# Kernel optimization log

Measured on AMD Instinct MI355X. Metric: run time of the kernel, lower is better.

The kernel has to match this reference:

```python
import jax, jax.numpy as jnp
import numpy as np

B, H, W, C = 2, 96, 96, 96
GROUPS = 32
EPS = 1e-5


def group_norm_dim1(x, gamma, beta):
    # Faithful to torch nn.GroupNorm(32, C) applied to an NHWC tensor:
    # dim 1 (H) is treated as the channel axis, normalized over (H//G, W, C) per group.
    b, h, w, c = x.shape
    xg = x.reshape(b, GROUPS, h // GROUPS, w, c)
    mean = xg.mean(axis=(2, 3, 4), keepdims=True)
    var = xg.var(axis=(2, 3, 4), keepdims=True)
    xn = ((xg - mean) * jax.lax.rsqrt(var + EPS)).reshape(b, h, w, c)
    return xn * gamma[None, :, None, None] + beta[None, :, None, None]


def setup_inputs() -> dict:
    key = jax.random.key(0)
    ks = jax.random.split(key, 9)
    s = 1.0 / np.sqrt(C)  # kaiming-uniform-ish scale
    x = jax.random.normal(ks[0], (B, H, W, C), dtype=jnp.float32)
    Wq = jax.random.uniform(ks[1], (C, C), jnp.float32, -s, s)
    Wk = jax.random.uniform(ks[2], (C, C), jnp.float32, -s, s)
    Wv = jax.random.uniform(ks[3], (C, C), jnp.float32, -s, s)
    Wp = jax.random.uniform(ks[4], (C, C), jnp.float32, -s, s)
    return {
        "x": x,
        "gamma": jnp.ones((H,), jnp.float32),   # GroupNorm affine weight (over dim 1)
        "beta": jnp.zeros((H,), jnp.float32),
        "Wq": Wq, "bq": jnp.zeros((C,), jnp.float32),
        "Wk": Wk, "bk": jnp.zeros((C,), jnp.float32),
        "Wv": Wv, "bv": jnp.zeros((C,), jnp.float32),
        "Wp": Wp, "bp": jnp.zeros((C,), jnp.float32),
    }


def reference(x, gamma, beta, Wq, bq, Wk, bk, Wv, bv, Wp, bp):
    b, h, w, c = x.shape
    hn = group_norm_dim1(x, gamma, beta)
    q = hn @ Wq + bq  # [B,H,W,C], Nin = contract last dim
    k = hn @ Wk + bk
    v = hn @ Wv + bv
    scale = c ** (-0.5)
    # full dense spatial attention: [B, HW, HW]
    scores = jnp.einsum('bxyc,buvc->bxyuv', q, k) * scale
    attn = jax.nn.softmax(scores.reshape(b, h, w, h * w), axis=-1).reshape(b, h, w, h, w)
    o = jnp.einsum('bxyuv,buvc->bxyc', attn, v)
    return x + (o @ Wp + bp)
```

## Files before the change

### kernel.cpp

```cpp
#include <hip/hip_runtime.h>
#include <hip/hip_bf16.h>
#include <stdint.h>

#define B_   2
#define H_   96
#define W_   96
#define C_   96
#define HW_  (H_ * W_)
#define NT_  (B_ * HW_)
#define EPS_ 1e-5f
#define KSPLIT  8
#define KRANGE  (HW_ / KSPLIT)
#define ATT_NIT (KRANGE / 32)
#define SCL (0.10206207261596575f * 1.4426950408889634f)

typedef __hip_bfloat16 bf16;
typedef __attribute__((ext_vector_type(8))) short short8;
typedef __attribute__((ext_vector_type(16))) float f32x16;

__device__ __forceinline__ uint32_t pk_bf16(float a, float b) {
    uint32_t ua = __float_as_uint(a) + 0x8000u;
    uint32_t ub = __float_as_uint(b) + 0x8000u;
    return __builtin_amdgcn_perm(ub, ua, 0x07060302u);
}
__device__ __forceinline__ float bl(uint32_t u) { uint32_t x = u << 16;         return *(float*)&x; }
__device__ __forceinline__ float bh(uint32_t u) { uint32_t x = u & 0xffff0000u; return *(float*)&x; }
__device__ __forceinline__ float fexp2(float x) { return __builtin_amdgcn_exp2f(x); }
__device__ __forceinline__ short8 lds_frag(const short* p) {
    union { int2 h[2]; short8 v; } t;
    t.h[0] = *(const int2*)(p);
    t.h[1] = *(const int2*)(p + 4);
    return t.v;
}

__device__ __forceinline__ void load_hn_frags(
        const float* __restrict__ x, const float2* __restrict__ stats,
        const float* __restrict__ gamma, const float* __restrict__ beta,
        int token, int hh, short8* hf) {
    int b = token / HW_;
    int h = (token % HW_) / W_;
    float2 st = stats[b * 32 + h / 3];
    float g0 = gamma[h];
    float ga = g0 * st.y;
    float be = beta[h] - st.x * st.y * g0;
    const float* xr = x + (size_t)token * C_ + hh * 8;
    #pragma unroll
    for (int s = 0; s < 6; ++s) {
        float4 a = *(const float4*)(xr + s * 16);
        float4 c = *(const float4*)(xr + s * 16 + 4);
        union { uint32_t w[4]; short8 v; } f;
        f.w[0] = pk_bf16(a.x * ga + be, a.y * ga + be);
        f.w[1] = pk_bf16(a.z * ga + be, a.w * ga + be);
        f.w[2] = pk_bf16(c.x * ga + be, c.y * ga + be);
        f.w[3] = pk_bf16(c.z * ga + be, c.w * ga + be);
        hf[s] = f.v;
    }
}

__global__ __launch_bounds__(1024)
void stats_prep_kernel(const float* __restrict__ x, float2* __restrict__ stats,
                       const float* __restrict__ Wq, const float* __restrict__ Wk,
                       const float* __restrict__ Wv, const float* __restrict__ Wp,
                       bf16* __restrict__ wqt, bf16* __restrict__ wkt,
                       bf16* __restrict__ wvt, bf16* __restrict__ wpt) {
    int blk = blockIdx.x;
    int tid = threadIdx.x;
    if (blk >= 64) {
        int wsel = blk - 64;
        const float* S = (wsel == 0) ? Wq : (wsel == 1) ? Wk : (wsel == 2) ? Wv : Wp;
        bf16* D = (wsel == 0) ? wqt : (wsel == 1) ? wkt : (wsel == 2) ? wvt : wpt;
        for (int i = tid; i < C_ * C_; i += 1024) {
            int r = i / C_, c = i % C_;
            D[c * C_ + r] = __float2bfloat16(S[r * C_ + c]);
        }
        return;
    }
    int b = blk >> 5, g = blk & 31;
    const int n4 = 3 * W_ * C_ / 4;
    const float4* xb = (const float4*)(x + (size_t)(b * H_ + 3 * g) * (W_ * C_));
    float s = 0.f, ss = 0.f;
    for (int i = tid; i < n4; i += 1024) {
        float4 v = xb[i];
        s  += v.x + v.y + v.z + v.w;
        ss += v.x * v.x + v.y * v.y + v.z * v.z + v.w * v.w;
    }
    #pragma unroll
    for (int off = 1; off < 64; off <<= 1) {
        s  += __shfl_xor(s, off, 64);
        ss += __shfl_xor(ss, off, 64);
    }
    __shared__ float rs[16], rss[16];
    int wid = tid >> 6;
    if ((tid & 63) == 0) { rs[wid] = s; rss[wid] = ss; }
    __syncthreads();
    if (tid == 0) {
        float ts = 0.f, tss = 0.f;
        #pragma unroll
        for (int i = 0; i < 16; ++i) { ts += rs[i]; tss += rss[i]; }
        const float n = 3 * W_ * C_;
        float mean = ts / n;
        float var  = tss / n - mean * mean;
        stats[blk] = make_float2(mean, rsqrtf(var + EPS_));
    }
}

__global__ __launch_bounds__(256)
void qkv_kernel(const float* __restrict__ x, const float2* __restrict__ stats,
                const float* __restrict__ gamma, const float* __restrict__ beta,
                const bf16* __restrict__ wqt, const bf16* __restrict__ wkt,
                const bf16* __restrict__ wvt,
                const float* __restrict__ bq, const float* __restrict__ bk,
                const float* __restrict__ bv,
                bf16* __restrict__ qb, bf16* __restrict__ kb, bf16* __restrict__ vt) {
    int blk = blockIdx.x;
    int w = blk / 144, grp = blk % 144;
    int wave = threadIdx.x >> 6, lane = threadIdx.x & 63;
    int tile = grp * 4 + wave;
    int n0 = tile * 32;
    int col = lane & 31, hh = lane >> 5;
    int token = n0 + col;

    short8 hf[6];
    load_hn_frags(x, stats, gamma, beta, token, hh, hf);

    if (w == 2) {
        int bb = n0 / HW_, nl0 = n0 % HW_;
        #pragma unroll
        for (int t = 0; t < 3; ++t) {
            int c = t * 32 + col;
            const bf16* wrow = wvt + (size_t)c * C_ + hh * 8;
            f32x16 acc = (f32x16)(0.f);
            #pragma unroll
            for (int s = 0; s < 6; ++s)
                acc = __builtin_amdgcn_mfma_f32_32x32x16_bf16(
                        hf[s], *(const short8*)(wrow + s * 16), acc, 0, 0, 0);
            float bias = bv[c];
            bf16* dst = vt + ((size_t)bb * C_ + c) * HW_ + nl0 + 4 * hh;
            #pragma unroll
            for (int g = 0; g < 4; ++g) {
                uint2 pk = make_uint2(pk_bf16(acc[4 * g] + bias, acc[4 * g + 1] + bias),
                                      pk_bf16(acc[4 * g + 2] + bias, acc[4 * g + 3] + bias));
                *(uint2*)(dst + 8 * g) = pk;
            }
        }
    } else {
        const bf16*  wt   = (w == 0) ? wqt : wkt;
        const float* bias = (w == 0) ? bq : bk;
        bf16*        dst  = (w == 0) ? qb : kb;
        float        scl  = (w == 0) ? SCL : 1.f;
        #pragma unroll
        for (int t = 0; t < 3; ++t) {
            const bf16* wrow = wt + (size_t)(t * 32 + col) * C_ + hh * 8;
            f32x16 acc = (f32x16)(0.f);
            #pragma unroll
            for (int s = 0; s < 6; ++s)
                acc = __builtin_amdgcn_mfma_f32_32x32x16_bf16(
                        *(const short8*)(wrow + s * 16), hf[s], acc, 0, 0, 0);
            #pragma unroll
            for (int g = 0; g < 4; ++g) {
                int nb = t * 32 + 8 * g + 4 * hh;
                float4 b4 = *(const float4*)(bias + nb);
                float v0 = (acc[4 * g]     + b4.x) * scl;
                float v1 = (acc[4 * g + 1] + b4.y) * scl;
                float v2 = (acc[4 * g + 2] + b4.z) * scl;
                float v3 = (acc[4 * g + 3] + b4.w) * scl;
                uint2 pk = make_uint2(pk_bf16(v0, v1), pk_bf16(v2, v3));
                *(uint2*)(dst + (size_t)token * C_ + nb) = pk;
            }
        }
    }
}

__global__ __launch_bounds__(256, 4)
void attn_kernel(const bf16* __restrict__ qb, const bf16* __restrict__ kb,
                 const bf16* __restrict__ vt,
                 bf16* __restrict__ pob, float* __restrict__ pl) {
    __shared__ short Kbuf[2][32 * 100];
    __shared__ short Vbuf[2][96 * 36];

    int blk = blockIdx.x;
    int ks = blk & 7, qg = blk >> 3;
    int b = qg / 72, g72 = qg % 72;
    int n0 = g72 * 128;
    int tid = threadIdx.x;
    int wave = tid >> 6, lane = tid & 63;
    int col = lane & 31, hh = lane >> 5;

    const bf16* kbb = kb + ((size_t)b * HW_ + (size_t)ks * KRANGE) * C_;
    const bf16* vbb = vt + (size_t)b * C_ * HW_ + (size_t)ks * KRANGE;

    int n = n0 + wave * 32 + col;
    short8 qf[6];
    {
        const bf16* qrow = qb + (size_t)(b * HW_ + n) * C_ + hh * 8;
        #pragma unroll
        for (int s = 0; s < 6; ++s) qf[s] = *(const short8*)(qrow + s * 16);
    }

    f32x16 oa[3];
    #pragma unroll
    for (int t = 0; t < 3; ++t) oa[t] = (f32x16)(0.f);
    float l_run = 0.f;

    bool isK = (tid < 128);
    int t128 = tid & 127;
    int ldsA[3], ldsB[3], goff[3];
    #pragma unroll
    for (int j = 0; j < 3; ++j) {
        int c = t128 + 128 * j;
        if (isK) {
            ldsA[j] = (c / 12) * 100 + (c % 12) * 8;
            ldsB[j] = ldsA[j] + 4;
            goff[j] = c * 8;
        } else {
            int rw = c >> 2, g = c & 3;
            ldsA[j] = rw * 36 + (2 * g - (g & 1)) * 4;
            ldsB[j] = rw * 36 + (2 * g + 2 - (g & 1)) * 4;
            goff[j] = rw * HW_ + g * 8;
        }
    }
    const bf16* gbase = isK ? kbb : vbb;
    const int itstep = isK ? (32 * C_) : 32;

    {
        short* sb = isK ? Kbuf[0] : Vbuf[0];
        #pragma unroll
        for (int j = 0; j < 3; ++j) {
            int4 r = *(const int4*)(gbase + goff[j]);
            *(int2*)(sb + ldsA[j]) = make_int2(r.x, r.y);
            *(int2*)(sb + ldsB[j]) = make_int2(r.z, r.w);
        }
    }
    __syncthreads();

    union FU { uint32_t w[4]; short8 v; };

    for (int it = 0; it < ATT_NIT; ++it) {
        int cur = it & 1;
        bool pre = (it + 1 < ATT_NIT);
        int4 r0, r1, r2;
        if (pre) {
            const bf16* g = gbase + (size_t)(it + 1) * itstep;
            r0 = *(const int4*)(g + goff[0]);
            r1 = *(const int4*)(g + goff[1]);
            r2 = *(const int4*)(g + goff[2]);
        }

        const short* Kc = Kbuf[cur];
        const short* Vc = Vbuf[cur];

        short8 kf[6];
        #pragma unroll
        for (int s = 0; s < 6; ++s)
            kf[s] = lds_frag(Kc + col * 100 + s * 16 + hh * 8);

        f32x16 st = (f32x16)(0.f);
        #pragma unroll
        for (int s = 0; s < 6; ++s)
            st = __builtin_amdgcn_mfma_f32_32x32x16_bf16(kf[s], qf[s], st, 0, 0, 0);

        float p[16], ls = 0.f;
        #pragma unroll
        for (int i = 0; i < 16; ++i) { p[i] = fexp2(st[i]); ls += p[i]; }
        l_run += ls;
        FU f0, f1;
        #pragma unroll
        for (int j = 0; j < 4; ++j) {
            f0.w[j] = pk_bf16(p[2 * j],     p[2 * j + 1]);
            f1.w[j] = pk_bf16(p[8 + 2 * j], p[8 + 2 * j + 1]);
        }

        #pragma unroll
        for (int t = 0; t < 3; ++t) {
            const short* vr = Vc + (32 * t + col) * 36 + hh * 8;
            short8 vf0 = lds_frag(vr);
            short8 vf1 = lds_frag(vr + 16);
            oa[t] = __builtin_amdgcn_mfma_f32_32x32x16_bf16(vf0, f0.v, oa[t], 0, 0, 0);
            oa[t] = __builtin_amdgcn_mfma_f32_32x32x16_bf16(vf1, f1.v, oa[t], 0, 0, 0);
        }

        if (pre) {
            short* sb = isK ? Kbuf[cur ^ 1] : Vbuf[cur ^ 1];
            *(int2*)(sb + ldsA[0]) = make_int2(r0.x, r0.y);
            *(int2*)(sb + ldsB[0]) = make_int2(r0.z, r0.w);
            *(int2*)(sb + ldsA[1]) = make_int2(r1.x, r1.y);
            *(int2*)(sb + ldsB[1]) = make_int2(r1.z, r1.w);
            *(int2*)(sb + ldsA[2]) = make_int2(r2.x, r2.y);
            *(int2*)(sb + ldsB[2]) = make_int2(r2.z, r2.w);
        }
        __syncthreads();
    }

    {
        size_t bq = (size_t)b * HW_ + n;
        float lt = l_run + __shfl_xor(l_run, 32, 64);
        if (hh == 0) pl[(size_t)ks * NT_ + bq] = lt;
        #pragma unroll
        for (int t = 0; t < 3; ++t)
            #pragma unroll
            for (int g = 0; g < 4; ++g) {
                int c0 = t * 32 + 8 * g + 4 * hh;
                uint2 pk = make_uint2(
                    pk_bf16(oa[t][4 * g],     oa[t][4 * g + 1]),
                    pk_bf16(oa[t][4 * g + 2], oa[t][4 * g + 3]));
                *(uint2*)(pob + ((size_t)ks * NT_ + bq) * C_ + c0) = pk;
            }
    }
}

__global__ __launch_bounds__(256)
void out_kernel(const float* __restrict__ x,
                const bf16* __restrict__ pob, const float* __restrict__ pl,
                const bf16* __restrict__ wpt, const float* __restrict__ bp,
                float* __restrict__ out) {
    __shared__ short ofs[32 * 100];
    __shared__ float linv_s[32];

    int tile = blockIdx.x;
    int n0 = tile * 32;
    int tid = threadIdx.x;

    if (tid < 32) {
        int token = n0 + tid;
        float l = 0.f;
        #pragma unroll
        for (int ksp = 0; ksp < KSPLIT; ++ksp) l += pl[(size_t)ksp * NT_ + token];
        linv_s[tid] = 1.f / l;
    }
    __syncthreads();

    for (int pos = tid; pos < 384; pos += 256) {
        int token = pos / 12, c8 = (pos % 12) * 8;
        float acc[8] = {0.f, 0.f, 0.f, 0.f, 0.f, 0.f, 0.f, 0.f};
        #pragma unroll
        for (int ksp = 0; ksp < KSPLIT; ++ksp) {
            uint4 u = *(const uint4*)(pob + ((size_t)ksp * NT_ + n0 + token) * C_ + c8);
            acc[0] += bl(u.x); acc[1] += bh(u.x);
            acc[2] += bl(u.y); acc[3] += bh(u.y);
            acc[4] += bl(u.z); acc[5] += bh(u.z);
            acc[6] += bl(u.w); acc[7] += bh(u.w);
        }
        float inv = linv_s[token];
        short* dst = ofs + token * 100 + c8;
        *(int2*)(dst)     = make_int2(pk_bf16(acc[0] * inv, acc[1] * inv),
                                      pk_bf16(acc[2] * inv, acc[3] * inv));
        *(int2*)(dst + 4) = make_int2(pk_bf16(acc[4] * inv, acc[5] * inv),
                                      pk_bf16(acc[6] * inv, acc[7] * inv));
    }
    __syncthreads();

    int wave = tid >> 6;
    if (wave >= 3) return;
    int lane = tid & 63, col = lane & 31, hh = lane >> 5;
    int t = wave;
    int token = n0 + col;

    short8 of[6];
    #pragma unroll
    for (int s = 0; s < 6; ++s)
        of[s] = lds_frag(ofs + col * 100 + s * 16 + hh * 8);

    f32x16 acc = (f32x16)(0.f);
    const bf16* wrow = wpt + (size_t)(t * 32 + col) * C_ + hh * 8;
    #pragma unroll
    for (int s = 0; s < 6; ++s)
        acc = __builtin_amdgcn_mfma_f32_32x32x16_bf16(
                *(const short8*)(wrow + s * 16), of[s], acc, 0, 0, 0);
    #pragma unroll
    for (int g = 0; g < 4; ++g) {
        int nb = t * 32 + 8 * g + 4 * hh;
        float4 b4 = *(const float4*)(bp + nb);
        float4 xv = *(const float4*)(x + (size_t)token * C_ + nb);
        float4 rr;
        rr.x = xv.x + acc[4 * g]     + b4.x;
        rr.y = xv.y + acc[4 * g + 1] + b4.y;
        rr.z = xv.z + acc[4 * g + 2] + b4.z;
        rr.w = xv.w + acc[4 * g + 3] + b4.w;
        *(float4*)(out + (size_t)token * C_ + nb) = rr;
    }
}

extern "C" void kernel_launch(void* const* d_in, const int* in_sizes, int n_in,
                              void* d_out, int out_size, void* d_ws, size_t ws_size,
                              hipStream_t stream) {
    const float* x     = (const float*)d_in[0];
    const float* gamma = (const float*)d_in[1];
    const float* beta  = (const float*)d_in[2];
    const float* Wq    = (const float*)d_in[3];
    const float* bq    = (const float*)d_in[4];
    const float* Wk    = (const float*)d_in[5];
    const float* bk    = (const float*)d_in[6];
    const float* Wv    = (const float*)d_in[7];
    const float* bv    = (const float*)d_in[8];
    const float* Wp    = (const float*)d_in[9];
    const float* bp    = (const float*)d_in[10];
    float* out = (float*)d_out;

    char* ws = (char*)d_ws;
    const size_t TB = (size_t)NT_ * C_ * 2;
    bf16* qb  = (bf16*)(ws);
    bf16* kb  = (bf16*)(ws + TB);
    bf16* vt  = (bf16*)(ws + 2 * TB);
    bf16* wqt = (bf16*)(ws + 3 * TB);
    bf16* wkt = (bf16*)(ws + 3 * TB + 18432);
    bf16* wvt = (bf16*)(ws + 3 * TB + 2 * 18432);
    bf16* wpt = (bf16*)(ws + 3 * TB + 3 * 18432);
    float2* stats = (float2*)(ws + 3 * TB + 4 * 18432);
    bf16*  pob = (bf16*)(ws + 3 * TB + 4 * 18432 + 512);
    float* pl  = (float*)(ws + 3 * TB + 4 * 18432 + 512
                          + (size_t)KSPLIT * NT_ * C_ * 2);

    hipLaunchKernelGGL(stats_prep_kernel, dim3(68), dim3(1024), 0, stream,
                       x, stats, Wq, Wk, Wv, Wp, wqt, wkt, wvt, wpt);
    hipLaunchKernelGGL(qkv_kernel, dim3(3 * 144), dim3(256), 0, stream,
                       x, stats, gamma, beta, wqt, wkt, wvt, bq, bk, bv, qb, kb, vt);
    hipLaunchKernelGGL(attn_kernel, dim3(1152), dim3(256), 0, stream,
                       qb, kb, vt, pob, pl);
    hipLaunchKernelGGL(out_kernel, dim3(576), dim3(256), 0, stream,
                       x, pob, pl, wpt, bp, out);
}
```

Baseline: 193.5 us.

## Fuse stats and QKV kernels via cooperative grid sync; split score MFMA chain

Merges the group-norm statistics/weight-transpose kernel and the QKV projection kernel into a single cooperative launch. Partial sums are written per block and combined after a grid-wide sync, and the stats pass is spread over 384 smaller blocks instead of 64 large ones. This removes one kernel launch boundary and improves parallelism in the stats pass, at the cost of a grid barrier and cooperative-launch constraints. Separately, the attention score MFMA chain is split into two independent accumulators to shorten the dependency chain.

```diff
diff --git a/kernel.cpp b/kernel.cpp
--- a/kernel.cpp
+++ b/kernel.cpp
@@ -1,6 +1,9 @@
 #include <hip/hip_runtime.h>
 #include <hip/hip_bf16.h>
+#include <hip/hip_cooperative_groups.h>
 #include <stdint.h>
+
+namespace cg = cooperative_groups;
 
 #define B_   2
 #define H_   96
@@ -33,95 +36,93 @@
     return t.v;
 }
 
-__device__ __forceinline__ void load_hn_frags(
-        const float* __restrict__ x, const float2* __restrict__ stats,
-        const float* __restrict__ gamma, const float* __restrict__ beta,
-        int token, int hh, short8* hf) {
-    int b = token / HW_;
-    int h = (token % HW_) / W_;
-    float2 st = stats[b * 32 + h / 3];
-    float g0 = gamma[h];
-    float ga = g0 * st.y;
-    float be = beta[h] - st.x * st.y * g0;
-    const float* xr = x + (size_t)token * C_ + hh * 8;
-    #pragma unroll
-    for (int s = 0; s < 6; ++s) {
-        float4 a = *(const float4*)(xr + s * 16);
-        float4 c = *(const float4*)(xr + s * 16 + 4);
-        union { uint32_t w[4]; short8 v; } f;
-        f.w[0] = pk_bf16(a.x * ga + be, a.y * ga + be);
-        f.w[1] = pk_bf16(a.z * ga + be, a.w * ga + be);
-        f.w[2] = pk_bf16(c.x * ga + be, c.y * ga + be);
-        f.w[3] = pk_bf16(c.z * ga + be, c.w * ga + be);
-        hf[s] = f.v;
-    }
-}
-
-__global__ __launch_bounds__(1024)
-void stats_prep_kernel(const float* __restrict__ x, float2* __restrict__ stats,
-                       const float* __restrict__ Wq, const float* __restrict__ Wk,
-                       const float* __restrict__ Wv, const float* __restrict__ Wp,
-                       bf16* __restrict__ wqt, bf16* __restrict__ wkt,
-                       bf16* __restrict__ wvt, bf16* __restrict__ wpt) {
+__global__ __launch_bounds__(256)
+void stats_qkv_kernel(const float* __restrict__ x,
+                      const float* __restrict__ gamma, const float* __restrict__ beta,
+                      const float* __restrict__ Wq, const float* __restrict__ Wk,
+                      const float* __restrict__ Wv, const float* __restrict__ Wp,
+                      bf16* __restrict__ wqt, bf16* __restrict__ wkt,
+                      bf16* __restrict__ wvt, bf16* __restrict__ wpt,
+                      const float* __restrict__ bq, const float* __restrict__ bk,
+                      const float* __restrict__ bv,
+                      bf16* __restrict__ qb, bf16* __restrict__ kb,
+                      bf16* __restrict__ vt, float2* __restrict__ pstats) {
     int blk = blockIdx.x;
     int tid = threadIdx.x;
-    if (blk >= 64) {
-        int wsel = blk - 64;
-        const float* S = (wsel == 0) ? Wq : (wsel == 1) ? Wk : (wsel == 2) ? Wv : Wp;
-        bf16* D = (wsel == 0) ? wqt : (wsel == 1) ? wkt : (wsel == 2) ? wvt : wpt;
-        for (int i = tid; i < C_ * C_; i += 1024) {
+
+    if (blk < 384) {
+        int g = blk / 6, part = blk % 6;
+        int b = g >> 5, gl = g & 31;
+        const float4* x4 = (const float4*)(x + (size_t)(b * H_ + 3 * gl) * (W_ * C_))
+                           + part * 1152;
+        float s = 0.f, ss = 0.f;
+        for (int i = tid; i < 1152; i += 256) {
+            float4 v = x4[i];
+            s  += v.x + v.y + v.z + v.w;
+            ss += v.x * v.x + v.y * v.y + v.z * v.z + v.w * v.w;
+        }
+        #pragma unroll
+        for (int off = 1; off < 64; off <<= 1) {
+            s  += __shfl_xor(s, off, 64);
+            ss += __shfl_xor(ss, off, 64);
+        }
+        __shared__ float rs[4], rss[4];
+        if ((tid & 63) == 0) { rs[tid >> 6] = s; rss[tid >> 6] = ss; }
+        __syncthreads();
+        if (tid == 0)
+            pstats[blk] = make_float2(rs[0] + rs[1] + rs[2] + rs[3],
+                                      rss[0] + rss[1] + rss[2] + rss[3]);
+    } else {
+        for (int e = (blk - 384) * 768 + tid; e < (blk - 384) * 768 + 768; e += 256) {
+            int w = e / 9216, i = e % 9216;
             int r = i / C_, c = i % C_;
+            const float* S = (w == 0) ? Wq : (w == 1) ? Wk : (w == 2) ? Wv : Wp;
+            bf16* D = (w == 0) ? wqt : (w == 1) ? wkt : (w == 2) ? wvt : wpt;
             D[c * C_ + r] = __float2bfloat16(S[r * C_ + c]);
         }
-        return;
-    }
-    int b = blk >> 5, g = blk & 31;
-    const int n4 = 3 * W_ * C_ / 4;
-    const float4* xb = (const float4*)(x + (size_t)(b * H_ + 3 * g) * (W_ * C_));
-    float s = 0.f, ss = 0.f;
-    for (int i = tid; i < n4; i += 1024) {
-        float4 v = xb[i];
-        s  += v.x + v.y + v.z + v.w;
-        ss += v.x * v.x + v.y * v.y + v.z * v.z + v.w * v.w;
-    }
-    #pragma unroll
-    for (int off = 1; off < 64; off <<= 1) {
-        s  += __shfl_xor(s, off, 64);
-        ss += __shfl_xor(ss, off, 64);
-    }
-    __shared__ float rs[16], rss[16];
-    int wid = tid >> 6;
-    if ((tid & 63) == 0) { rs[wid] = s; rss[wid] = ss; }
-    __syncthreads();
-    if (tid == 0) {
-        float ts = 0.f, tss = 0.f;
-        #pragma unroll
-        for (int i = 0; i < 16; ++i) { ts += rs[i]; tss += rss[i]; }
-        const float n = 3 * W_ * C_;
-        float mean = ts / n;
-        float var  = tss / n - mean * mean;
-        stats[blk] = make_float2(mean, rsqrtf(var + EPS_));
-    }
-}
-
-__global__ __launch_bounds__(256)
-void qkv_kernel(const float* __restrict__ x, const float2* __restrict__ stats,
-                const float* __restrict__ gamma, const float* __restrict__ beta,
-                const bf16* __restrict__ wqt, const bf16* __restrict__ wkt,
-                const bf16* __restrict__ wvt,
-                const float* __restrict__ bq, const float* __restrict__ bk,
-                const float* __restrict__ bv,
-                bf16* __restrict__ qb, bf16* __restrict__ kb, bf16* __restrict__ vt) {
-    int blk = blockIdx.x;
+    }
+
+    __threadfence();
+    cg::this_grid().sync();
+
     int w = blk / 144, grp = blk % 144;
-    int wave = threadIdx.x >> 6, lane = threadIdx.x & 63;
+    int wave = tid >> 6, lane = tid & 63;
     int tile = grp * 4 + wave;
     int n0 = tile * 32;
     int col = lane & 31, hh = lane >> 5;
     int token = n0 + col;
 
+    int bb0 = token / HW_;
+    int h = (token % HW_) / W_;
+    float mean, rstd;
+    {
+        const float2* ps = pstats + (bb0 * 32 + h / 3) * 6;
+        float ts = 0.f, tss = 0.f;
+        #pragma unroll
+        for (int i = 0; i < 6; ++i) { float2 p2 = ps[i]; ts += p2.x; tss += p2.y; }
+        const float inv_n = 1.f / (3 * W_ * C_);
+        mean = ts * inv_n;
+        rstd = rsqrtf(tss * inv_n - mean * mean + EPS_);
+    }
+    float g0 = gamma[h];
+    float ga = g0 * rstd;
+    float be = beta[h] - mean * rstd * g0;
+
     short8 hf[6];
-    load_hn_frags(x, stats, gamma, beta, token, hh, hf);
+    {
+        const float* xr = x + (size_t)token * C_ + hh * 8;
+        #pragma unroll
+        for (int s = 0; s < 6; ++s) {
+            float4 a = *(const float4*)(xr + s * 16);
+            float4 c = *(const float4*)(xr + s * 16 + 4);
+            union { uint32_t w[4]; short8 v; } f;
+            f.w[0] = pk_bf16(a.x * ga + be, a.y * ga + be);
+            f.w[1] = pk_bf16(a.z * ga + be, a.w * ga + be);
+            f.w[2] = pk_bf16(c.x * ga + be, c.y * ga + be);
+            f.w[3] = pk_bf16(c.z * ga + be, c.w * ga + be);
+            hf[s] = f.v;
+        }
+    }
 
     if (w == 2) {
         int bb = n0 / HW_, nl0 = n0 % HW_;
@@ -254,14 +255,16 @@
         for (int s = 0; s < 6; ++s)
             kf[s] = lds_frag(Kc + col * 100 + s * 16 + hh * 8);
 
-        f32x16 st = (f32x16)(0.f);
-        #pragma unroll
-        for (int s = 0; s < 6; ++s)
-            st = __builtin_amdgcn_mfma_f32_32x32x16_bf16(kf[s], qf[s], st, 0, 0, 0);
+        f32x16 sa = (f32x16)(0.f), sb2 = (f32x16)(0.f);
+        #pragma unroll
+        for (int s = 0; s < 3; ++s) {
+            sa  = __builtin_amdgcn_mfma_f32_32x32x16_bf16(kf[s],     qf[s],     sa,  0, 0, 0);
+            sb2 = __builtin_amdgcn_mfma_f32_32x32x16_bf16(kf[s + 3], qf[s + 3], sb2, 0, 0, 0);
+        }
 
         float p[16], ls = 0.f;
         #pragma unroll
-        for (int i = 0; i < 16; ++i) { p[i] = fexp2(st[i]); ls += p[i]; }
+        for (int i = 0; i < 16; ++i) { p[i] = fexp2(sa[i] + sb2[i]); ls += p[i]; }
         l_run += ls;
         FU f0, f1;
         #pragma unroll
@@ -405,15 +408,19 @@
     bf16* wkt = (bf16*)(ws + 3 * TB + 18432);
     bf16* wvt = (bf16*)(ws + 3 * TB + 2 * 18432);
     bf16* wpt = (bf16*)(ws + 3 * TB + 3 * 18432);
-    float2* stats = (float2*)(ws + 3 * TB + 4 * 18432);
-    bf16*  pob = (bf16*)(ws + 3 * TB + 4 * 18432 + 512);
-    float* pl  = (float*)(ws + 3 * TB + 4 * 18432 + 512
+    float2* pstats = (float2*)(ws + 3 * TB + 4 * 18432);
+    bf16*  pob = (bf16*)(ws + 3 * TB + 4 * 18432 + 4096);
+    float* pl  = (float*)(ws + 3 * TB + 4 * 18432 + 4096
                           + (size_t)KSPLIT * NT_ * C_ * 2);
 
-    hipLaunchKernelGGL(stats_prep_kernel, dim3(68), dim3(1024), 0, stream,
-                       x, stats, Wq, Wk, Wv, Wp, wqt, wkt, wvt, wpt);
-    hipLaunchKernelGGL(qkv_kernel, dim3(3 * 144), dim3(256), 0, stream,
-                       x, stats, gamma, beta, wqt, wkt, wvt, bq, bk, bv, qb, kb, vt);
+    void* args[] = { (void*)&x, (void*)&gamma, (void*)&beta,
+                     (void*)&Wq, (void*)&Wk, (void*)&Wv, (void*)&Wp,
+                     (void*)&wqt, (void*)&wkt, (void*)&wvt, (void*)&wpt,
+                     (void*)&bq, (void*)&bk, (void*)&bv,
+                     (void*)&qb, (void*)&kb, (void*)&vt, (void*)&pstats };
+    hipLaunchCooperativeKernel((const void*)stats_qkv_kernel,
+                               dim3(432), dim3(256), args, 0, stream);
+
     hipLaunchKernelGGL(attn_kernel, dim3(1152), dim3(256), 0, stream,
                        qb, kb, vt, pob, pl);
     hipLaunchKernelGGL(out_kernel, dim3(576), dim3(256), 0, stream,
```

Result: slower. 299.9 us (+55.0%).
